# Kernel tuning notes

Measured on AMD Instinct MI355X. Metric: run time of the kernel, lower is better.

The kernel has to match this reference:

```python
import jax, jax.numpy as jnp
import numpy as np

RATE = 0.001  # matches init kwarg `rate`


def _hebbian_layer(vi, w, b, c1w, c1b, c2w, c2b, batch_num):
    # vi: (B, I), w: (O, I), b: (O,)
    vj = jax.nn.relu(vi @ w.T + b)  # (B, O) == relu(old_vj)
    # meta-MLP over the broadcasted (B, O, I) grid with 3 input channels
    # (input_stack, weight_stack, output_stack); conv1 is 1x1 so it is a
    # per-element linear map 3 -> H. We fuse the broadcast into the matmul
    # instead of materializing the stacked (B, 3, O, I) tensor.
    # c1w: (H, 3), c1b: (H,)
    h = jax.nn.relu(
        vi[:, None, :, None] * c1w[:, 0]
        + w[None, :, :, None] * c1w[:, 1]
        + vj[:, :, None, None] * c1w[:, 2]
        + c1b
    )  # (B, O, I, H)
    # conv2: H -> 1, then squeeze; scale by rate / batch_num
    shift = (h @ c2w + c2b) * (RATE / batch_num)  # (B, O, I)
    # out = old_vj + sum(input_stack * shift, dim=2)
    out = vj + jnp.sum(vi[:, None, :] * shift, axis=2)  # (B, O)
    # NOTE: torch also does layer.data += mean(shift, dim=0) as a stateful
    # side effect; it does not affect this forward pass's return value.
    return out


def setup_inputs() -> dict:
    key = jax.random.key(0)
    ks = jax.random.split(key, 9)
    B, I, Hd, O, MH = 8, 1024, 2048, 512, 8
    inp = {
        "x": jax.random.normal(ks[0], (B, I), dtype=jnp.float32),
        "w1": jax.random.normal(ks[1], (Hd, I), dtype=jnp.float32) * 0.02,
        "b1": jax.random.normal(ks[2], (Hd,), dtype=jnp.float32) * 0.02,
        "w2": jax.random.normal(ks[3], (O, Hd), dtype=jnp.float32) * 0.02,
        "b2": jax.random.normal(ks[4], (O,), dtype=jnp.float32) * 0.02,
        "c1w": jax.random.normal(ks[5], (MH, 3), dtype=jnp.float32) * 0.5,
        "c1b": jax.random.normal(ks[6], (MH,), dtype=jnp.float32) * 0.5,
        "c2w": jax.random.normal(ks[7], (MH,), dtype=jnp.float32) * 0.5,
        "c2b": jax.random.normal(ks[8], (), dtype=jnp.float32) * 0.5,
        "batch_num": 1,
    }
    return inp


def reference(x, w1, b1, w2, b2, c1w, c1b, c2w, c2b, batch_num):
    out = _hebbian_layer(x, w1, b1, c1w, c1b, c2w, c2b, batch_num)
    out = _hebbian_layer(out, w2, b2, c1w, c1b, c2w, c2b, batch_num)
    return out
```

## Files before the change

### kernel.cpp

```cpp
#include <hip/hip_runtime.h>

#define RATE 0.001f

template<int I>
__global__ __launch_bounds__(256) void hebb_layer(
    const float* __restrict__ vi,
    const float* __restrict__ w,
    const float* __restrict__ bias,
    const float* __restrict__ c1w,
    const float* __restrict__ c1b,
    const float* __restrict__ c2w,
    const float* __restrict__ c2b_p,
    const int*   __restrict__ bn_p,
    float* __restrict__ out,
    int O)
{
    const int o    = blockIdx.x;
    const int tid  = threadIdx.x;
    const int lane = tid & 63;
    const int wid  = tid >> 6;

    __shared__ float red[4][16];
    __shared__ float s_vj[8];
    __shared__ float s_S[8];

    float p[8], q[8], r[8], cb[8], c2[8];
#pragma unroll
    for (int h = 0; h < 8; ++h) {
        p[h]  = c1w[h * 3 + 0];
        q[h]  = c1w[h * 3 + 1];
        r[h]  = c1w[h * 3 + 2];
        cb[h] = c1b[h];
        c2[h] = c2w[h];
    }
    const float c2b   = *c2b_p;
    const float scale = RATE / (float)(*bn_p);
    const float bo    = bias[o];
    const float* __restrict__ wrow = w + (size_t)o * I;

    float dot[8], ss[8];
#pragma unroll
    for (int b = 0; b < 8; ++b) { dot[b] = 0.f; ss[b] = 0.f; }

    for (int i = tid; i < I; i += 256) {
        const float wv = wrow[i];
#pragma unroll
        for (int b = 0; b < 8; ++b) {
            const float a = vi[b * I + i];
            dot[b] = fmaf(a, wv, dot[b]);
            ss[b] += a;
        }
    }
#pragma unroll
    for (int b = 0; b < 8; ++b) {
#pragma unroll
        for (int off = 32; off; off >>= 1) {
            dot[b] += __shfl_down(dot[b], off, 64);
            ss[b]  += __shfl_down(ss[b],  off, 64);
        }
    }
    if (lane == 0) {
#pragma unroll
        for (int b = 0; b < 8; ++b) { red[wid][b] = dot[b]; red[wid][8 + b] = ss[b]; }
    }
    __syncthreads();
    if (tid < 8) {
        const float d = red[0][tid] + red[1][tid] + red[2][tid] + red[3][tid];
        const float s = red[0][8 + tid] + red[1][8 + tid] + red[2][8 + tid] + red[3][8 + tid];
        s_vj[tid] = fmaxf(d + bo, 0.f);
        s_S[tid]  = s;
    }
    __syncthreads();

    float k[8][8];
#pragma unroll
    for (int b = 0; b < 8; ++b) {
        const float v = s_vj[b];
#pragma unroll
        for (int h = 0; h < 8; ++h) k[b][h] = fmaf(v, r[h], cb[h]);
    }

    float acc[8];
#pragma unroll
    for (int b = 0; b < 8; ++b) acc[b] = 0.f;

    for (int i = tid; i < I; i += 256) {
        const float wv = wrow[i];
        float m[8];
#pragma unroll
        for (int h = 0; h < 8; ++h) m[h] = wv * q[h];
        float a[8];
#pragma unroll
        for (int b = 0; b < 8; ++b) a[b] = vi[b * I + i];
#pragma unroll
        for (int b = 0; b < 8; ++b) {
            float t = 0.f;
#pragma unroll
            for (int h = 0; h < 8; ++h) {
                const float u = fmaxf(fmaf(a[b], p[h], m[h] + k[b][h]), 0.f);
                t = fmaf(u, c2[h], t);
            }
            acc[b] = fmaf(a[b], t, acc[b]);
        }
    }

#pragma unroll
    for (int b = 0; b < 8; ++b) {
#pragma unroll
        for (int off = 32; off; off >>= 1) acc[b] += __shfl_down(acc[b], off, 64);
    }
    __syncthreads();
    if (lane == 0) {
#pragma unroll
        for (int b = 0; b < 8; ++b) red[wid][b] = acc[b];
    }
    __syncthreads();
    if (tid < 8) {
        const float rsum = red[0][tid] + red[1][tid] + red[2][tid] + red[3][tid];
        out[tid * O + o] = s_vj[tid] + scale * (rsum + c2b * s_S[tid]);
    }
}

extern "C" void kernel_launch(void* const* d_in, const int* in_sizes, int n_in,
                              void* d_out, int out_size, void* d_ws, size_t ws_size,
                              hipStream_t stream) {
    const float* x   = (const float*)d_in[0];
    const float* w1  = (const float*)d_in[1];
    const float* b1  = (const float*)d_in[2];
    const float* w2  = (const float*)d_in[3];
    const float* b2  = (const float*)d_in[4];
    const float* c1w = (const float*)d_in[5];
    const float* c1b = (const float*)d_in[6];
    const float* c2w = (const float*)d_in[7];
    const float* c2b = (const float*)d_in[8];
    const int*   bn  = (const int*)d_in[9];

    float* out = (float*)d_out;
    float* mid = (float*)d_ws;

    hebb_layer<1024><<<2048, 256, 0, stream>>>(x,   w1, b1, c1w, c1b, c2w, c2b, bn, mid, 2048);
    hebb_layer<2048><<<512,  256, 0, stream>>>(mid, w2, b2, c1w, c1b, c2w, c2b, bn, out, 512);
}
```

Before: 119.7 us.

## Assign batch pairs per wavefront with packed-float2 math and vector loads

```diff
diff --git a/kernel.cpp b/kernel.cpp
--- a/kernel.cpp
+++ b/kernel.cpp
@@ -1,6 +1,11 @@
 #include <hip/hip_runtime.h>
 
 #define RATE 0.001f
+
+typedef float f2 __attribute__((ext_vector_type(2)));
+typedef float f4 __attribute__((ext_vector_type(4)));
+
+static __device__ __forceinline__ f2 splat2(float v) { f2 r; r.x = v; r.y = v; return r; }
 
 template<int I>
 __global__ __launch_bounds__(256) void hebb_layer(
@@ -19,105 +24,96 @@
     const int tid  = threadIdx.x;
     const int lane = tid & 63;
     const int wid  = tid >> 6;
+    const int b0   = wid * 2;
 
-    __shared__ float red[4][16];
-    __shared__ float s_vj[8];
-    __shared__ float s_S[8];
-
-    float p[8], q[8], r[8], cb[8], c2[8];
+    f2 p2[4], q2[4], r2[4], cb2[4], c22[4];
 #pragma unroll
-    for (int h = 0; h < 8; ++h) {
-        p[h]  = c1w[h * 3 + 0];
-        q[h]  = c1w[h * 3 + 1];
-        r[h]  = c1w[h * 3 + 2];
-        cb[h] = c1b[h];
-        c2[h] = c2w[h];
+    for (int j = 0; j < 4; ++j) {
+        p2[j].x  = c1w[(2*j)*3 + 0];  p2[j].y  = c1w[(2*j+1)*3 + 0];
+        q2[j].x  = c1w[(2*j)*3 + 1];  q2[j].y  = c1w[(2*j+1)*3 + 1];
+        r2[j].x  = c1w[(2*j)*3 + 2];  r2[j].y  = c1w[(2*j+1)*3 + 2];
+        cb2[j].x = c1b[2*j];          cb2[j].y = c1b[2*j+1];
+        c22[j].x = c2w[2*j];          c22[j].y = c2w[2*j+1];
     }
     const float c2b   = *c2b_p;
     const float scale = RATE / (float)(*bn_p);
     const float bo    = bias[o];
-    const float* __restrict__ wrow = w + (size_t)o * I;
 
-    float dot[8], ss[8];
+    const float* __restrict__ wrow  = w  + (size_t)o  * I;
+    const float* __restrict__ arow0 = vi + (size_t)b0 * I;
+    const float* __restrict__ arow1 = arow0 + I;
+
+    constexpr int ITERS = I / 256;
+
+    float dot0 = 0.f, dot1 = 0.f, ss0 = 0.f, ss1 = 0.f;
+    for (int it = 0; it < ITERS; ++it) {
+        const int base = it * 256 + lane * 4;
+        const f4 wv = *(const f4*)(wrow  + base);
+        const f4 a0 = *(const f4*)(arow0 + base);
+        const f4 a1 = *(const f4*)(arow1 + base);
 #pragma unroll
-    for (int b = 0; b < 8; ++b) { dot[b] = 0.f; ss[b] = 0.f; }
-
-    for (int i = tid; i < I; i += 256) {
-        const float wv = wrow[i];
-#pragma unroll
-        for (int b = 0; b < 8; ++b) {
-            const float a = vi[b * I + i];
-            dot[b] = fmaf(a, wv, dot[b]);
-            ss[b] += a;
+        for (int e = 0; e < 4; ++e) {
+            dot0 = fmaf(a0[e], wv[e], dot0);
+            dot1 = fmaf(a1[e], wv[e], dot1);
+            ss0 += a0[e];
+            ss1 += a1[e];
         }
     }
 #pragma unroll
-    for (int b = 0; b < 8; ++b) {
+    for (int off = 1; off < 64; off <<= 1) {
+        dot0 += __shfl_xor(dot0, off, 64);
+        dot1 += __shfl_xor(dot1, off, 64);
+        ss0  += __shfl_xor(ss0,  off, 64);
+        ss1  += __shfl_xor(ss1,  off, 64);
+    }
+    const float vj0 = fmaxf(dot0 + bo, 0.f);
+    const float vj1 = fmaxf(dot1 + bo, 0.f);
+
+    f2 k20[4], k21[4];
 #pragma unroll
-        for (int off = 32; off; off >>= 1) {
-            dot[b] += __shfl_down(dot[b], off, 64);
-            ss[b]  += __shfl_down(ss[b],  off, 64);
+    for (int j = 0; j < 4; ++j) {
+        k20[j] = splat2(vj0) * r2[j] + cb2[j];
+        k21[j] = splat2(vj1) * r2[j] + cb2[j];
+    }
+
+    f2 acc0 = splat2(0.f), acc1 = splat2(0.f);
+    for (int it = 0; it < ITERS; ++it) {
+        const int base = it * 256 + lane * 4;
+        const f4 wv4 = *(const f4*)(wrow  + base);
+        const f4 a04 = *(const f4*)(arow0 + base);
+        const f4 a14 = *(const f4*)(arow1 + base);
+#pragma unroll
+        for (int e = 0; e < 4; ++e) {
+            const f2 wvE = splat2(wv4[e]);
+            const f2 a0E = splat2(a04[e]);
+            const f2 a1E = splat2(a14[e]);
+            f2 t0 = splat2(0.f), t1 = splat2(0.f);
+#pragma unroll
+            for (int j = 0; j < 4; ++j) {
+                f2 z0 = wvE * q2[j] + k20[j];
+                z0 = a0E * p2[j] + z0;
+                const f2 u0 = __builtin_elementwise_max(z0, splat2(0.f));
+                t0 = u0 * c22[j] + t0;
+                f2 z1 = wvE * q2[j] + k21[j];
+                z1 = a1E * p2[j] + z1;
+                const f2 u1 = __builtin_elementwise_max(z1, splat2(0.f));
+                t1 = u1 * c22[j] + t1;
+            }
+            acc0 = a0E * t0 + acc0;
+            acc1 = a1E * t1 + acc1;
         }
     }
-    if (lane == 0) {
+    float r0 = acc0.x + acc0.y;
+    float r1 = acc1.x + acc1.y;
 #pragma unroll
-        for (int b = 0; b < 8; ++b) { red[wid][b] = dot[b]; red[wid][8 + b] = ss[b]; }
-    }
-    __syncthreads();
-    if (tid < 8) {
-        const float d = red[0][tid] + red[1][tid] + red[2][tid] + red[3][tid];
-        const float s = red[0][8 + tid] + red[1][8 + tid] + red[2][8 + tid] + red[3][8 + tid];
-        s_vj[tid] = fmaxf(d + bo, 0.f);
-        s_S[tid]  = s;
-    }
-    __syncthreads();
-
-    float k[8][8];
-#pragma unroll
-    for (int b = 0; b < 8; ++b) {
-        const float v = s_vj[b];
-#pragma unroll
-        for (int h = 0; h < 8; ++h) k[b][h] = fmaf(v, r[h], cb[h]);
+    for (int off = 1; off < 64; off <<= 1) {
+        r0 += __shfl_xor(r0, off, 64);
+        r1 += __shfl_xor(r1, off, 64);
     }
 
-    float acc[8];
-#pragma unroll
-    for (int b = 0; b < 8; ++b) acc[b] = 0.f;
-
-    for (int i = tid; i < I; i += 256) {
-        const float wv = wrow[i];
-        float m[8];
-#pragma unroll
-        for (int h = 0; h < 8; ++h) m[h] = wv * q[h];
-        float a[8];
-#pragma unroll
-        for (int b = 0; b < 8; ++b) a[b] = vi[b * I + i];
-#pragma unroll
-        for (int b = 0; b < 8; ++b) {
-            float t = 0.f;
-#pragma unroll
-            for (int h = 0; h < 8; ++h) {
-                const float u = fmaxf(fmaf(a[b], p[h], m[h] + k[b][h]), 0.f);
-                t = fmaf(u, c2[h], t);
-            }
-            acc[b] = fmaf(a[b], t, acc[b]);
-        }
-    }
-
-#pragma unroll
-    for (int b = 0; b < 8; ++b) {
-#pragma unroll
-        for (int off = 32; off; off >>= 1) acc[b] += __shfl_down(acc[b], off, 64);
-    }
-    __syncthreads();
     if (lane == 0) {
-#pragma unroll
-        for (int b = 0; b < 8; ++b) red[wid][b] = acc[b];
-    }
-    __syncthreads();
-    if (tid < 8) {
-        const float rsum = red[0][tid] + red[1][tid] + red[2][tid] + red[3][tid];
-        out[tid * O + o] = s_vj[tid] + scale * (rsum + c2b * s_S[tid]);
+        out[(size_t)(b0    ) * O + o] = vj0 + scale * (r0 + c2b * ss0);
+        out[(size_t)(b0 + 1) * O + o] = vj1 + scale * (r1 + c2b * ss1);
     }
 }
 
```

New measurement: 102.9 us. -14.1%, faster.
